# Optimization experiments

Measured on AMD Instinct MI355X. Metric: run time of the kernel, lower is better.

The kernel has to match this reference:

```python
import jax, jax.numpy as jnp
import numpy as np

NSTATE = 1024


def setup_inputs() -> dict:
    key = jax.random.key(0)
    ks = jax.random.split(key, 10)
    b, t = 128, 512
    nalpha, nemb, n = 128, 256, NSTATE
    s = 0.02
    return {
        "x": jax.random.randint(ks[0], (b, t), 0, nalpha),
        "emb": jax.random.normal(ks[1], (nalpha, nemb), jnp.float32) * s,
        "W_fi": jax.random.normal(ks[2], (nemb + 2 * n, 2 * n), jnp.float32) * s,
        "b_fi": jnp.zeros((2 * n,), jnp.float32),
        "W_cu": jax.random.normal(ks[3], (nemb + n, n), jnp.float32) * s,
        "b_cu": jnp.zeros((n,), jnp.float32),
        "W_h": jax.random.normal(ks[4], (nemb + 2 * n, n), jnp.float32) * s,
        "b_h": jnp.zeros((n,), jnp.float32),
        "W_out": jax.random.normal(ks[5], (n, nalpha), jnp.float32) * s,
        "b_out": jnp.zeros((nalpha,), jnp.float32),
    }


def reference(x, emb, W_fi, b_fi, W_cu, b_cu, W_h, b_h, W_out, b_out):
    b, t = x.shape
    n = NSTATE
    f = emb[x]                      # (b, t, nemb) embedding lookup
    f_t = jnp.transpose(f, (1, 0, 2))  # (t, b, nemb) for scan over time

    def step(carry, xt):
        h, c = carry
        ga = jnp.concatenate([xt, h, c], axis=1)        # (b, nemb+2n)
        fi = jax.nn.sigmoid(ga @ W_fi + b_fi)           # (b, 2n) forget|input
        cu = jnp.tanh(jnp.concatenate([xt, h], axis=1) @ W_cu + b_cu)
        c2 = fi[:, :n] * c + fi[:, n:] * cu             # (b, n)
        hg = jnp.concatenate([xt, h, c2], axis=1) @ W_h + b_h  # note: no sigmoid (faithful to source)
        h2 = hg * jnp.tanh(c2)
        return (h2, c2), h2

    init = (jnp.zeros((b, n), f.dtype), jnp.zeros((b, n), f.dtype))
    _, states_t = jax.lax.scan(step, init, f_t)         # (t, b, n)
    states = jnp.transpose(states_t, (1, 0, 2))         # (b, t, n)
    y = states @ W_out + b_out                          # (b, t, nalphabet)
    return y
```

## Files before the change

kernel.cpp:

```cpp
#include <hip/hip_runtime.h>

typedef __attribute__((ext_vector_type(8))) short short8;
typedef __attribute__((ext_vector_type(4))) float f32x4;

#define B_   128
#define T_   512
#define NE_  256
#define N_   1024
#define NA_  128
#define KFI  2304
#define KCU  1280
#define BN   (B_ * N_)
#define TS   513

#define OFF_WTFI   0UL
#define OFF_WTCU   9437184UL
#define OFF_WTH    12058624UL
#define OFF_WTOUT  16777216UL
#define OFF_XE     17039360UL
#define OFF_FLAGS  50593792UL
#define OFF_CBF    50595840UL
#define OFF_STATES 51120128UL

__device__ __forceinline__ unsigned short f2bf(float v) {
  unsigned int u = __float_as_uint(v);
  unsigned int r = (u + 0x7fffu + ((u >> 16) & 1u)) >> 16;
  return (unsigned short)r;
}
__device__ __forceinline__ float sigm(float x) { return 1.f / (1.f + __expf(-x)); }
__device__ __forceinline__ float tanhfast(float x) { return 1.f - 2.f / (__expf(2.f * x) + 1.f); }

#define MFMA(a, b, c) __builtin_amdgcn_mfma_f32_16x16x32_bf16((a), (b), (c), 0, 0, 0)

__device__ __forceinline__ short8 ld8_agent(const unsigned short* p) {
  union { unsigned long long q[2]; short8 v; } u;
  u.q[0] = __hip_atomic_load((unsigned long long*)p,     __ATOMIC_RELAXED, __HIP_MEMORY_SCOPE_AGENT);
  u.q[1] = __hip_atomic_load((unsigned long long*)p + 1, __ATOMIC_RELAXED, __HIP_MEMORY_SCOPE_AGENT);
  return u.v;
}

__global__ void transpose_to_bf16(const float* __restrict__ src,
                                  unsigned short* __restrict__ dst,
                                  int K, int N) {
  __shared__ float tile[32][33];
  const int k0 = blockIdx.y * 32, n0 = blockIdx.x * 32;
  const int tx = threadIdx.x, ty = threadIdx.y;
#pragma unroll
  for (int i = 0; i < 32; i += 8)
    tile[ty + i][tx] = src[(size_t)(k0 + ty + i) * N + n0 + tx];
  __syncthreads();
#pragma unroll
  for (int i = 0; i < 32; i += 8)
    dst[(size_t)(n0 + ty + i) * K + k0 + tx] = f2bf(tile[tx][ty + i]);
}

__global__ void embed_kernel(const int* __restrict__ x, const float* __restrict__ emb,
                             unsigned short* __restrict__ xe) {
  const int r = blockIdx.x;
  const int b = r & 127, t = r >> 7;
  const int e = threadIdx.x;
  const int a = x[b * T_ + t];
  xe[(size_t)r * NE_ + e] = f2bf(emb[(size_t)a * NE_ + e]);
}

__global__ void zero_sync_region(char* __restrict__ ws) {
  unsigned* p = (unsigned*)(ws + OFF_FLAGS);
  const int i = blockIdx.x * blockDim.x + threadIdx.x;
  if (i < (int)((OFF_STATES - OFF_FLAGS) / 4))
    __hip_atomic_store(p + i, 0u, __ATOMIC_RELAXED, __HIP_MEMORY_SCOPE_AGENT);
}

__global__ void zero_h0(char* __restrict__ ws) {
  unsigned* st = (unsigned*)(ws + OFF_STATES);
  unsigned* row = st + (size_t)blockIdx.x * TS * 512;
  __hip_atomic_store(row + threadIdx.x,       0u, __ATOMIC_RELAXED, __HIP_MEMORY_SCOPE_AGENT);
  __hip_atomic_store(row + 256 + threadIdx.x, 0u, __ATOMIC_RELAXED, __HIP_MEMORY_SCOPE_AGENT);
}

__global__ void __launch_bounds__(256) lstm_persistent(
    char* __restrict__ ws,
    const float* __restrict__ b_fi,
    const float* __restrict__ b_cu,
    const float* __restrict__ b_h) {
  const unsigned short* Wt_fi = (const unsigned short*)(ws + OFF_WTFI);
  const unsigned short* Wt_cu = (const unsigned short*)(ws + OFF_WTCU);
  const unsigned short* Wt_h  = (const unsigned short*)(ws + OFF_WTH);
  const unsigned short* xe    = (const unsigned short*)(ws + OFF_XE);
  unsigned short* cbf = (unsigned short*)(ws + OFF_CBF);
  unsigned*       cbf32 = (unsigned*)(ws + OFF_CBF);
  unsigned short* states = (unsigned short*)(ws + OFF_STATES);
  unsigned*       states32 = (unsigned*)(ws + OFF_STATES);
  unsigned* flagsP = (unsigned*)(ws + OFF_FLAGS);
  unsigned* flagsQ = flagsP + 256;

  const int blk  = blockIdx.x;
  const int xcd  = blk & 7;
  const int slot = blk >> 3;
  const int ni   = xcd * 8 + (slot >> 2);
  const int mi   = slot & 3;
  const int tid  = threadIdx.x;
  const int wave = tid >> 6;
  const int lane = tid & 63;
  const int l15  = lane & 15;
  const int quad = lane >> 4;
  const int qo   = quad * 8;
  const int n0   = ni * 16;
  const int mA0  = mi * 32 + l15;
  const int mA1  = mA0 + 16;

  const unsigned short* bfp = Wt_fi + (size_t)(n0 + l15) * KFI;
  const unsigned short* bip = Wt_fi + (size_t)(N_ + n0 + l15) * KFI;
  const unsigned short* bup = Wt_cu + (size_t)(n0 + l15) * KCU;
  const unsigned short* bhp = Wt_h  + (size_t)(n0 + l15) * KFI;

  unsigned* gflagP = flagsP + mi * 64;
  unsigned* gflagQ = flagsQ + mi * 64;

  __shared__ float red[4][6][4][64];
  __shared__ float sb[4][16];
  if (tid < 64) {
    const int g = tid >> 4, col = tid & 15;
    float v;
    if      (g == 0) v = b_fi[n0 + col];
    else if (g == 1) v = b_fi[N_ + n0 + col];
    else if (g == 2) v = b_cu[n0 + col];
    else             v = b_h[n0 + col];
    sb[g][col] = v;
  }

  const int row_l = tid >> 3;
  const int colp  = tid & 7;
  const int gh    = row_l >> 4;
  const int re    = row_l & 3;
  const int lbase = ((row_l >> 2) & 3) * 16 + colp * 2;
  const int me    = mi * 32 + row_l;

  float creg[2] = {0.f, 0.f};

  for (int t = 0; t < T_; ++t) {
    const int cur = t & 1, prv = cur ^ 1;
    const unsigned short* xr0 = xe + ((size_t)t * B_ + mA0) * NE_;
    const unsigned short* xr1 = xe + ((size_t)t * B_ + mA1) * NE_;
    const unsigned short* hr0 = states + ((size_t)mA0 * TS + t) * N_;
    const unsigned short* hr1 = states + ((size_t)mA1 * TS + t) * N_;
    const unsigned short* cr0 = cbf + (size_t)prv * BN + (size_t)mA0 * N_;
    const unsigned short* cr1 = cbf + (size_t)prv * BN + (size_t)mA1 * N_;

    if (wave == 0) {
      const unsigned tgt = (unsigned)t;
      while (__hip_atomic_load(gflagQ + lane, __ATOMIC_RELAXED, __HIP_MEMORY_SCOPE_AGENT) < tgt) { }
    }
    __syncthreads();
    __builtin_amdgcn_fence(__ATOMIC_ACQUIRE, "workgroup");

    short8 axh0[10], axh1[10];
    f32x4 f0 = {0.f,0.f,0.f,0.f}, f1 = {0.f,0.f,0.f,0.f};
    f32x4 i0 = {0.f,0.f,0.f,0.f}, i1 = {0.f,0.f,0.f,0.f};
    f32x4 u0 = {0.f,0.f,0.f,0.f}, u1 = {0.f,0.f,0.f,0.f};
#pragma unroll
    for (int c = 0; c < 10; ++c) {
      const int k = (wave + 4 * c) * 32;
      short8 a0, a1;
      if (c < 2) {
        a0 = *(const short8*)(xr0 + k + qo);
        a1 = *(const short8*)(xr1 + k + qo);
      } else {
        a0 = __builtin_nontemporal_load((const short8*)(hr0 + (k - NE_) + qo));
        a1 = __builtin_nontemporal_load((const short8*)(hr1 + (k - NE_) + qo));
      }
      axh0[c] = a0; axh1[c] = a1;
      short8 bf = *(const short8*)(bfp + k + qo);
      short8 bi = *(const short8*)(bip + k + qo);
      short8 bu = *(const short8*)(bup + k + qo);
      f0 = MFMA(a0, bf, f0);  f1 = MFMA(a1, bf, f1);
      i0 = MFMA(a0, bi, i0);  i1 = MFMA(a1, bi, i1);
      u0 = MFMA(a0, bu, u0);  u1 = MFMA(a1, bu, u1);
    }
#pragma unroll
    for (int c = 10; c < 18; ++c) {
      const int k = (wave + 4 * c) * 32;
      short8 a0 = ld8_agent(cr0 + (k - NE_ - N_) + qo);
      short8 a1 = ld8_agent(cr1 + (k - NE_ - N_) + qo);
      short8 bf = *(const short8*)(bfp + k + qo);
      short8 bi = *(const short8*)(bip + k + qo);
      f0 = MFMA(a0, bf, f0);  f1 = MFMA(a1, bf, f1);
      i0 = MFMA(a0, bi, i0);  i1 = MFMA(a1, bi, i1);
    }
#pragma unroll
    for (int r = 0; r < 4; ++r) {
      red[wave][0][r][lane] = f0[r];  red[wave][1][r][lane] = f1[r];
      red[wave][2][r][lane] = i0[r];  red[wave][3][r][lane] = i1[r];
      red[wave][4][r][lane] = u0[r];  red[wave][5][r][lane] = u1[r];
    }
    __syncthreads();
    {
      unsigned pack = 0;
#pragma unroll
      for (int j = 0; j < 2; ++j) {
        const int L = lbase + j;
        const float fv = red[0][gh][re][L] + red[1][gh][re][L] +
                         red[2][gh][re][L] + red[3][gh][re][L] + sb[0][colp * 2 + j];
        const float iv = red[0][2+gh][re][L] + red[1][2+gh][re][L] +
                         red[2][2+gh][re][L] + red[3][2+gh][re][L] + sb[1][colp * 2 + j];
        const float uv = red[0][4+gh][re][L] + red[1][4+gh][re][L] +
                         red[2][4+gh][re][L] + red[3][4+gh][re][L] + sb[2][colp * 2 + j];
        const float c2v = sigm(fv) * creg[j] + sigm(iv) * tanhfast(uv);
        creg[j] = c2v;
        pack |= (unsigned)f2bf(c2v) << (16 * j);
      }
      unsigned* p = cbf32 + (((size_t)cur * BN + (size_t)me * N_ + n0 + colp * 2) >> 1);
      __hip_atomic_store(p, pack, __ATOMIC_RELAXED, __HIP_MEMORY_SCOPE_AGENT);
    }
    __builtin_amdgcn_fence(__ATOMIC_RELEASE, "workgroup");
    __builtin_amdgcn_s_waitcnt(0);
    __syncthreads();
    if (tid == 0)
      __hip_atomic_store(gflagP + ni, (unsigned)(t + 1), __ATOMIC_RELAXED, __HIP_MEMORY_SCOPE_AGENT);

    f32x4 h0 = {0.f,0.f,0.f,0.f}, h1 = {0.f,0.f,0.f,0.f};
#pragma unroll
    for (int c = 0; c < 10; ++c) {
      const int k = (wave + 4 * c) * 32;
      short8 bh = *(const short8*)(bhp + k + qo);
      h0 = MFMA(axh0[c], bh, h0);
      h1 = MFMA(axh1[c], bh, h1);
    }
    if (wave == 0) {
      const unsigned tgt = (unsigned)(t + 1);
      while (__hip_atomic_load(gflagP + lane, __ATOMIC_RELAXED, __HIP_MEMORY_SCOPE_AGENT) < tgt) { }
    }
    __syncthreads();
    __builtin_amdgcn_fence(__ATOMIC_ACQUIRE, "workgroup");
    const unsigned short* c2r0 = cbf + (size_t)cur * BN + (size_t)mA0 * N_;
    const unsigned short* c2r1 = cbf + (size_t)cur * BN + (size_t)mA1 * N_;
#pragma unroll
    for (int c = 10; c < 18; ++c) {
      const int k = (wave + 4 * c) * 32;
      short8 a0 = ld8_agent(c2r0 + (k - NE_ - N_) + qo);
      short8 a1 = ld8_agent(c2r1 + (k - NE_ - N_) + qo);
      short8 bh = *(const short8*)(bhp + k + qo);
      h0 = MFMA(a0, bh, h0);
      h1 = MFMA(a1, bh, h1);
    }
#pragma unroll
    for (int r = 0; r < 4; ++r) {
      red[wave][0][r][lane] = h0[r];
      red[wave][1][r][lane] = h1[r];
    }
    __syncthreads();
    {
      unsigned pack = 0;
#pragma unroll
      for (int j = 0; j < 2; ++j) {
        const int L = lbase + j;
        const float hv = red[0][gh][re][L] + red[1][gh][re][L] +
                         red[2][gh][re][L] + red[3][gh][re][L] + sb[3][colp * 2 + j];
        const float h2 = hv * tanhfast(creg[j]);
        pack |= (unsigned)f2bf(h2) << (16 * j);
      }
      unsigned* p = states32 + (((size_t)me * TS + t + 1) * N_ + n0 + colp * 2 >> 1);
      __hip_atomic_store(p, pack, __ATOMIC_RELAXED, __HIP_MEMORY_SCOPE_AGENT);
    }
    __builtin_amdgcn_fence(__ATOMIC_RELEASE, "workgroup");
    __builtin_amdgcn_s_waitcnt(0);
    __syncthreads();
    if (tid == 0)
      __hip_atomic_store(gflagQ + ni, (unsigned)(t + 1), __ATOMIC_RELAXED, __HIP_MEMORY_SCOPE_AGENT);
  }
}

__global__ void __launch_bounds__(256) out_gemm(const char* __restrict__ ws,
                                                const float* __restrict__ b_out,
                                                float* __restrict__ y) {
  const unsigned short* states = (const unsigned short*)(ws + OFF_STATES);
  const unsigned short* Wt_out = (const unsigned short*)(ws + OFF_WTOUT);
  const int tid = threadIdx.x, wave = tid >> 6, lane = tid & 63;
  const int l15 = lane & 15, quad = lane >> 4, qo = quad * 8;
  const int msub = wave & 1, npair = wave >> 1;
  const size_t r0 = (size_t)blockIdx.x * 32;
  const size_t mb = r0 >> 9;
  const unsigned short* arow =
      states + (mb * TS + (r0 & 511) + msub * 16 + l15 + 1) * N_;
  const unsigned short* b0p = Wt_out + (size_t)(npair * 64 + 0  + l15) * N_;
  const unsigned short* b1p = Wt_out + (size_t)(npair * 64 + 16 + l15) * N_;
  const unsigned short* b2p = Wt_out + (size_t)(npair * 64 + 32 + l15) * N_;
  const unsigned short* b3p = Wt_out + (size_t)(npair * 64 + 48 + l15) * N_;
  f32x4 a0 = {0.f,0.f,0.f,0.f}, a1 = {0.f,0.f,0.f,0.f};
  f32x4 a2 = {0.f,0.f,0.f,0.f}, a3 = {0.f,0.f,0.f,0.f};
#pragma unroll 8
  for (int c = 0; c < 32; ++c) {
    const int k = c * 32;
    short8 av = *(const short8*)(arow + k + qo);
    a0 = MFMA(av, *(const short8*)(b0p + k + qo), a0);
    a1 = MFMA(av, *(const short8*)(b1p + k + qo), a1);
    a2 = MFMA(av, *(const short8*)(b2p + k + qo), a2);
    a3 = MFMA(av, *(const short8*)(b3p + k + qo), a3);
  }
#pragma unroll
  for (int r = 0; r < 4; ++r) {
    const size_t m = r0 + msub * 16 + quad * 4 + r;
    y[m * NA_ + npair * 64 + 0  + l15] = a0[r] + b_out[npair * 64 + 0  + l15];
    y[m * NA_ + npair * 64 + 16 + l15] = a1[r] + b_out[npair * 64 + 16 + l15];
    y[m * NA_ + npair * 64 + 32 + l15] = a2[r] + b_out[npair * 64 + 32 + l15];
    y[m * NA_ + npair * 64 + 48 + l15] = a3[r] + b_out[npair * 64 + 48 + l15];
  }
}

extern "C" void kernel_launch(void* const* d_in, const int* in_sizes, int n_in,
                              void* d_out, int out_size, void* d_ws, size_t ws_size,
                              hipStream_t stream) {
  const int*   x     = (const int*)d_in[0];
  const float* emb   = (const float*)d_in[1];
  const float* W_fi  = (const float*)d_in[2];
  const float* b_fi  = (const float*)d_in[3];
  const float* W_cu  = (const float*)d_in[4];
  const float* b_cu  = (const float*)d_in[5];
  const float* W_h   = (const float*)d_in[6];
  const float* b_h   = (const float*)d_in[7];
  const float* W_out = (const float*)d_in[8];
  const float* b_out = (const float*)d_in[9];
  char* ws = (char*)d_ws;
  float* y = (float*)d_out;
  (void)in_sizes; (void)n_in; (void)out_size; (void)ws_size;

  transpose_to_bf16<<<dim3(2048 / 32, 2304 / 32), dim3(32, 8), 0, stream>>>(
      W_fi, (unsigned short*)(ws + OFF_WTFI), KFI, 2048);
  transpose_to_bf16<<<dim3(1024 / 32, 1280 / 32), dim3(32, 8), 0, stream>>>(
      W_cu, (unsigned short*)(ws + OFF_WTCU), KCU, 1024);
  transpose_to_bf16<<<dim3(1024 / 32, 2304 / 32), dim3(32, 8), 0, stream>>>(
      W_h, (unsigned short*)(ws + OFF_WTH), KFI, 1024);
  transpose_to_bf16<<<dim3(128 / 32, 1024 / 32), dim3(32, 8), 0, stream>>>(
      W_out, (unsigned short*)(ws + OFF_WTOUT), N_, 128);

  embed_kernel<<<T_ * B_, NE_, 0, stream>>>(x, emb, (unsigned short*)(ws + OFF_XE));

  zero_sync_region<<<514, 256, 0, stream>>>(ws);
  zero_h0<<<128, 256, 0, stream>>>(ws);

  char* wsp = ws;
  void* kargs[4] = { (void*)&wsp, (void*)&b_fi, (void*)&b_cu, (void*)&b_h };
  hipLaunchCooperativeKernel((void*)lstm_persistent, dim3(256), dim3(256),
                             kargs, 0, stream);

  out_gemm<<<(B_ * T_) / 32, 256, 0, stream>>>(ws, b_out, y);
}
```

Baseline: 10.66 ms.

## Split batch into two interleaved 16-row groups to overlap sync waits with compute

Each block now handles two independent 16-row batch groups instead of one 32-row group. It interleaves their P (cell) and Q (hidden) phases, so the MFMA work of one group can run while the other group's flags propagate. Within each phase, the loads that do not depend on the flag (x, c, or h) are issued before the spin-wait, which moves useful work ahead of the synchronization point. The cost is twice as many flag waits and barriers per step with smaller MFMA batches per phase. The explicit acquire/release fences are also removed, which leaves memory-ordering correctness resting on waitcnt and agent-scope atomics.

Result: slower. 17.58 ms (+65.0%).

```diff
diff --git a/kernel.cpp b/kernel.cpp
--- a/kernel.cpp
+++ b/kernel.cpp
@@ -19,8 +19,8 @@
 #define OFF_WTOUT  16777216UL
 #define OFF_XE     17039360UL
 #define OFF_FLAGS  50593792UL
-#define OFF_CBF    50595840UL
-#define OFF_STATES 51120128UL
+#define OFF_CBF    50597888UL
+#define OFF_STATES 51122176UL
 
 __device__ __forceinline__ unsigned short f2bf(float v) {
   unsigned int u = __float_as_uint(v);
@@ -86,18 +86,19 @@
   const unsigned short* Wt_cu = (const unsigned short*)(ws + OFF_WTCU);
   const unsigned short* Wt_h  = (const unsigned short*)(ws + OFF_WTH);
   const unsigned short* xe    = (const unsigned short*)(ws + OFF_XE);
-  unsigned short* cbf = (unsigned short*)(ws + OFF_CBF);
-  unsigned*       cbf32 = (unsigned*)(ws + OFF_CBF);
+  unsigned short* cbf    = (unsigned short*)(ws + OFF_CBF);
+  unsigned*       cbf32  = (unsigned*)(ws + OFF_CBF);
   unsigned short* states = (unsigned short*)(ws + OFF_STATES);
   unsigned*       states32 = (unsigned*)(ws + OFF_STATES);
-  unsigned* flagsP = (unsigned*)(ws + OFF_FLAGS);
-  unsigned* flagsQ = flagsP + 256;
+  unsigned* fP = (unsigned*)(ws + OFF_FLAGS);
+  unsigned* fQ = fP + 512;
 
   const int blk  = blockIdx.x;
   const int xcd  = blk & 7;
-  const int slot = blk >> 3;
-  const int ni   = xcd * 8 + (slot >> 2);
-  const int mi   = slot & 3;
+  const int slot = (blk >> 3) & 3;
+  const int nh   = blk >> 5;
+  const int ni   = xcd * 8 + nh;
+  const int gA   = slot, gB = slot + 4;
   const int tid  = threadIdx.x;
   const int wave = tid >> 6;
   const int lane = tid & 63;
@@ -105,18 +106,13 @@
   const int quad = lane >> 4;
   const int qo   = quad * 8;
   const int n0   = ni * 16;
-  const int mA0  = mi * 32 + l15;
-  const int mA1  = mA0 + 16;
 
   const unsigned short* bfp = Wt_fi + (size_t)(n0 + l15) * KFI;
   const unsigned short* bip = Wt_fi + (size_t)(N_ + n0 + l15) * KFI;
   const unsigned short* bup = Wt_cu + (size_t)(n0 + l15) * KCU;
   const unsigned short* bhp = Wt_h  + (size_t)(n0 + l15) * KFI;
 
-  unsigned* gflagP = flagsP + mi * 64;
-  unsigned* gflagQ = flagsQ + mi * 64;
-
-  __shared__ float red[4][6][4][64];
+  __shared__ float red[4][3][4][72];
   __shared__ float sb[4][16];
   if (tid < 64) {
     const int g = tid >> 4, col = tid & 15;
@@ -128,144 +124,138 @@
     sb[g][col] = v;
   }
 
-  const int row_l = tid >> 3;
-  const int colp  = tid & 7;
-  const int gh    = row_l >> 4;
-  const int re    = row_l & 3;
-  const int lbase = ((row_l >> 2) & 3) * 16 + colp * 2;
-  const int me    = mi * 32 + row_l;
-
-  float creg[2] = {0.f, 0.f};
+  const int erow = tid >> 3;
+  const int colp = tid & 7;
+  const int ereg = erow & 3;
+  const int lbas = (erow >> 2) * 16 + colp * 2;
+
+  float cA[2] = {0.f, 0.f}, cB[2] = {0.f, 0.f};
+
+  auto phaseP = [&](const int g, const int t, float* cv) {
+    const int cur = t & 1, prv = cur ^ 1;
+    const unsigned short* xr = xe + ((size_t)t * B_ + g * 16 + l15) * NE_;
+    const unsigned short* hr = states + ((size_t)(g * 16 + l15) * TS + t) * N_;
+    const unsigned short* cr = cbf + (size_t)prv * BN + (size_t)(g * 16 + l15) * N_;
+    f32x4 fa = {0.f,0.f,0.f,0.f}, ia = {0.f,0.f,0.f,0.f}, ua = {0.f,0.f,0.f,0.f};
+#pragma unroll
+    for (int c = 0; c < 2; ++c) {
+      const int k = (wave + 4 * c) * 32;
+      short8 a = *(const short8*)(xr + k + qo);
+      fa = MFMA(a, *(const short8*)(bfp + k + qo), fa);
+      ia = MFMA(a, *(const short8*)(bip + k + qo), ia);
+      ua = MFMA(a, *(const short8*)(bup + k + qo), ua);
+    }
+#pragma unroll
+    for (int c = 10; c < 18; ++c) {
+      const int k = (wave + 4 * c) * 32;
+      short8 a = ld8_agent(cr + (k - KCU) + qo);
+      fa = MFMA(a, *(const short8*)(bfp + k + qo), fa);
+      ia = MFMA(a, *(const short8*)(bip + k + qo), ia);
+    }
+    if (wave == 0) {
+      while (__hip_atomic_load(fQ + g * 64 + lane, __ATOMIC_RELAXED,
+                               __HIP_MEMORY_SCOPE_AGENT) < (unsigned)t) { }
+    }
+    __syncthreads();
+#pragma unroll
+    for (int c = 2; c < 10; ++c) {
+      const int k = (wave + 4 * c) * 32;
+      short8 a = __builtin_nontemporal_load((const short8*)(hr + (k - NE_) + qo));
+      fa = MFMA(a, *(const short8*)(bfp + k + qo), fa);
+      ia = MFMA(a, *(const short8*)(bip + k + qo), ia);
+      ua = MFMA(a, *(const short8*)(bup + k + qo), ua);
+    }
+#pragma unroll
+    for (int r = 0; r < 4; ++r) {
+      red[wave][0][r][lane] = fa[r];
+      red[wave][1][r][lane] = ia[r];
+      red[wave][2][r][lane] = ua[r];
+    }
+    __syncthreads();
+    if (tid < 128) {
+      unsigned pack = 0;
+#pragma unroll
+      for (int j = 0; j < 2; ++j) {
+        const int L = lbas + j;
+        const float fv = red[0][0][ereg][L] + red[1][0][ereg][L] +
+                         red[2][0][ereg][L] + red[3][0][ereg][L] + sb[0][colp * 2 + j];
+        const float iv = red[0][1][ereg][L] + red[1][1][ereg][L] +
+                         red[2][1][ereg][L] + red[3][1][ereg][L] + sb[1][colp * 2 + j];
+        const float uv = red[0][2][ereg][L] + red[1][2][ereg][L] +
+                         red[2][2][ereg][L] + red[3][2][ereg][L] + sb[2][colp * 2 + j];
+        const float c2 = sigm(fv) * cv[j] + sigm(iv) * tanhfast(uv);
+        cv[j] = c2;
+        pack |= (unsigned)f2bf(c2) << (16 * j);
+      }
+      unsigned* p = cbf32 +
+          (((size_t)cur * BN + (size_t)(g * 16 + erow) * N_ + n0 + colp * 2) >> 1);
+      __hip_atomic_store(p, pack, __ATOMIC_RELAXED, __HIP_MEMORY_SCOPE_AGENT);
+    }
+    __builtin_amdgcn_s_waitcnt(0);
+    __syncthreads();
+    if (tid == 0)
+      __hip_atomic_store(fP + g * 64 + ni, (unsigned)(t + 1), __ATOMIC_RELAXED,
+                         __HIP_MEMORY_SCOPE_AGENT);
+  };
+
+  auto phaseQ = [&](const int g, const int t, const float* cv) {
+    const int cur = t & 1;
+    const unsigned short* xr = xe + ((size_t)t * B_ + g * 16 + l15) * NE_;
+    const unsigned short* hr = states + ((size_t)(g * 16 + l15) * TS + t) * N_;
+    const unsigned short* c2r = cbf + (size_t)cur * BN + (size_t)(g * 16 + l15) * N_;
+    f32x4 ha = {0.f,0.f,0.f,0.f};
+#pragma unroll
+    for (int c = 0; c < 2; ++c) {
+      const int k = (wave + 4 * c) * 32;
+      short8 a = *(const short8*)(xr + k + qo);
+      ha = MFMA(a, *(const short8*)(bhp + k + qo), ha);
+    }
+#pragma unroll
+    for (int c = 2; c < 10; ++c) {
+      const int k = (wave + 4 * c) * 32;
+      short8 a = __builtin_nontemporal_load((const short8*)(hr + (k - NE_) + qo));
+      ha = MFMA(a, *(const short8*)(bhp + k + qo), ha);
+    }
+    if (wave == 0) {
+      while (__hip_atomic_load(fP + g * 64 + lane, __ATOMIC_RELAXED,
+                               __HIP_MEMORY_SCOPE_AGENT) < (unsigned)(t + 1)) { }
+    }
+    __syncthreads();
+#pragma unroll
+    for (int c = 10; c < 18; ++c) {
+      const int k = (wave + 4 * c) * 32;
+      short8 a = ld8_agent(c2r + (k - KCU) + qo);
+      ha = MFMA(a, *(const short8*)(bhp + k + qo), ha);
+    }
+#pragma unroll
+    for (int r = 0; r < 4; ++r)
+      red[wave][0][r][lane] = ha[r];
+    __syncthreads();
+    if (tid < 128) {
+      unsigned pack = 0;
+#pragma unroll
+      for (int j = 0; j < 2; ++j) {
+        const int L = lbas + j;
+        const float hv = red[0][0][ereg][L] + red[1][0][ereg][L] +
+                         red[2][0][ereg][L] + red[3][0][ereg][L] + sb[3][colp * 2 + j];
+        pack |= (unsigned)f2bf(hv * tanhfast(cv[j])) << (16 * j);
+      }
+      unsigned* p = states32 +
+          ((((size_t)(g * 16 + erow) * TS + (t + 1)) * N_ + n0 + colp * 2) >> 1);
+      __hip_atomic_store(p, pack, __ATOMIC_RELAXED, __HIP_MEMORY_SCOPE_AGENT);
+    }
+    __builtin_amdgcn_s_waitcnt(0);
+    __syncthreads();
+    if (tid == 0)
+      __hip_atomic_store(fQ + g * 64 + ni, (unsigned)(t + 1), __ATOMIC_RELAXED,
+                         __HIP_MEMORY_SCOPE_AGENT);
+  };
 
   for (int t = 0; t < T_; ++t) {
-    const int cur = t & 1, prv = cur ^ 1;
-    const unsigned short* xr0 = xe + ((size_t)t * B_ + mA0) * NE_;
-    const unsigned short* xr1 = xe + ((size_t)t * B_ + mA1) * NE_;
-    const unsigned short* hr0 = states + ((size_t)mA0 * TS + t) * N_;
-    const unsigned short* hr1 = states + ((size_t)mA1 * TS + t) * N_;
-    const unsigned short* cr0 = cbf + (size_t)prv * BN + (size_t)mA0 * N_;
-    const unsigned short* cr1 = cbf + (size_t)prv * BN + (size_t)mA1 * N_;
-
-    if (wave == 0) {
-      const unsigned tgt = (unsigned)t;
-      while (__hip_atomic_load(gflagQ + lane, __ATOMIC_RELAXED, __HIP_MEMORY_SCOPE_AGENT) < tgt) { }
-    }
-    __syncthreads();
-    __builtin_amdgcn_fence(__ATOMIC_ACQUIRE, "workgroup");
-
-    short8 axh0[10], axh1[10];
-    f32x4 f0 = {0.f,0.f,0.f,0.f}, f1 = {0.f,0.f,0.f,0.f};
-    f32x4 i0 = {0.f,0.f,0.f,0.f}, i1 = {0.f,0.f,0.f,0.f};
-    f32x4 u0 = {0.f,0.f,0.f,0.f}, u1 = {0.f,0.f,0.f,0.f};
-#pragma unroll
-    for (int c = 0; c < 10; ++c) {
-      const int k = (wave + 4 * c) * 32;
-      short8 a0, a1;
-      if (c < 2) {
-        a0 = *(const short8*)(xr0 + k + qo);
-        a1 = *(const short8*)(xr1 + k + qo);
-      } else {
-        a0 = __builtin_nontemporal_load((const short8*)(hr0 + (k - NE_) + qo));
-        a1 = __builtin_nontemporal_load((const short8*)(hr1 + (k - NE_) + qo));
-      }
-      axh0[c] = a0; axh1[c] = a1;
-      short8 bf = *(const short8*)(bfp + k + qo);
-      short8 bi = *(const short8*)(bip + k + qo);
-      short8 bu = *(const short8*)(bup + k + qo);
-      f0 = MFMA(a0, bf, f0);  f1 = MFMA(a1, bf, f1);
-      i0 = MFMA(a0, bi, i0);  i1 = MFMA(a1, bi, i1);
-      u0 = MFMA(a0, bu, u0);  u1 = MFMA(a1, bu, u1);
-    }
-#pragma unroll
-    for (int c = 10; c < 18; ++c) {
-      const int k = (wave + 4 * c) * 32;
-      short8 a0 = ld8_agent(cr0 + (k - NE_ - N_) + qo);
-      short8 a1 = ld8_agent(cr1 + (k - NE_ - N_) + qo);
-      short8 bf = *(const short8*)(bfp + k + qo);
-      short8 bi = *(const short8*)(bip + k + qo);
-      f0 = MFMA(a0, bf, f0);  f1 = MFMA(a1, bf, f1);
-      i0 = MFMA(a0, bi, i0);  i1 = MFMA(a1, bi, i1);
-    }
-#pragma unroll
-    for (int r = 0; r < 4; ++r) {
-      red[wave][0][r][lane] = f0[r];  red[wave][1][r][lane] = f1[r];
-      red[wave][2][r][lane] = i0[r];  red[wave][3][r][lane] = i1[r];
-      red[wave][4][r][lane] = u0[r];  red[wave][5][r][lane] = u1[r];
-    }
-    __syncthreads();
-    {
-      unsigned pack = 0;
-#pragma unroll
-      for (int j = 0; j < 2; ++j) {
-        const int L = lbase + j;
-        const float fv = red[0][gh][re][L] + red[1][gh][re][L] +
-                         red[2][gh][re][L] + red[3][gh][re][L] + sb[0][colp * 2 + j];
-        const float iv = red[0][2+gh][re][L] + red[1][2+gh][re][L] +
-                         red[2][2+gh][re][L] + red[3][2+gh][re][L] + sb[1][colp * 2 + j];
-        const float uv = red[0][4+gh][re][L] + red[1][4+gh][re][L] +
-                         red[2][4+gh][re][L] + red[3][4+gh][re][L] + sb[2][colp * 2 + j];
-        const float c2v = sigm(fv) * creg[j] + sigm(iv) * tanhfast(uv);
-        creg[j] = c2v;
-        pack |= (unsigned)f2bf(c2v) << (16 * j);
-      }
-      unsigned* p = cbf32 + (((size_t)cur * BN + (size_t)me * N_ + n0 + colp * 2) >> 1);
-      __hip_atomic_store(p, pack, __ATOMIC_RELAXED, __HIP_MEMORY_SCOPE_AGENT);
-    }
-    __builtin_amdgcn_fence(__ATOMIC_RELEASE, "workgroup");
-    __builtin_amdgcn_s_waitcnt(0);
-    __syncthreads();
-    if (tid == 0)
-      __hip_atomic_store(gflagP + ni, (unsigned)(t + 1), __ATOMIC_RELAXED, __HIP_MEMORY_SCOPE_AGENT);
-
-    f32x4 h0 = {0.f,0.f,0.f,0.f}, h1 = {0.f,0.f,0.f,0.f};
-#pragma unroll
-    for (int c = 0; c < 10; ++c) {
-      const int k = (wave + 4 * c) * 32;
-      short8 bh = *(const short8*)(bhp + k + qo);
-      h0 = MFMA(axh0[c], bh, h0);
-      h1 = MFMA(axh1[c], bh, h1);
-    }
-    if (wave == 0) {
-      const unsigned tgt = (unsigned)(t + 1);
-      while (__hip_atomic_load(gflagP + lane, __ATOMIC_RELAXED, __HIP_MEMORY_SCOPE_AGENT) < tgt) { }
-    }
-    __syncthreads();
-    __builtin_amdgcn_fence(__ATOMIC_ACQUIRE, "workgroup");
-    const unsigned short* c2r0 = cbf + (size_t)cur * BN + (size_t)mA0 * N_;
-    const unsigned short* c2r1 = cbf + (size_t)cur * BN + (size_t)mA1 * N_;
-#pragma unroll
-    for (int c = 10; c < 18; ++c) {
-      const int k = (wave + 4 * c) * 32;
-      short8 a0 = ld8_agent(c2r0 + (k - NE_ - N_) + qo);
-      short8 a1 = ld8_agent(c2r1 + (k - NE_ - N_) + qo);
-      short8 bh = *(const short8*)(bhp + k + qo);
-      h0 = MFMA(a0, bh, h0);
-      h1 = MFMA(a1, bh, h1);
-    }
-#pragma unroll
-    for (int r = 0; r < 4; ++r) {
-      red[wave][0][r][lane] = h0[r];
-      red[wave][1][r][lane] = h1[r];
-    }
-    __syncthreads();
-    {
-      unsigned pack = 0;
-#pragma unroll
-      for (int j = 0; j < 2; ++j) {
-        const int L = lbase + j;
-        const float hv = red[0][gh][re][L] + red[1][gh][re][L] +
-                         red[2][gh][re][L] + red[3][gh][re][L] + sb[3][colp * 2 + j];
-        const float h2 = hv * tanhfast(creg[j]);
-        pack |= (unsigned)f2bf(h2) << (16 * j);
-      }
-      unsigned* p = states32 + (((size_t)me * TS + t + 1) * N_ + n0 + colp * 2 >> 1);
-      __hip_atomic_store(p, pack, __ATOMIC_RELAXED, __HIP_MEMORY_SCOPE_AGENT);
-    }
-    __builtin_amdgcn_fence(__ATOMIC_RELEASE, "workgroup");
-    __builtin_amdgcn_s_waitcnt(0);
-    __syncthreads();
-    if (tid == 0)
-      __hip_atomic_store(gflagQ + ni, (unsigned)(t + 1), __ATOMIC_RELAXED, __HIP_MEMORY_SCOPE_AGENT);
+    phaseP(gA, t, cA);
+    phaseP(gB, t, cB);
+    phaseQ(gA, t, cA);
+    phaseQ(gB, t, cB);
   }
 }
 
@@ -334,7 +324,7 @@
 
   embed_kernel<<<T_ * B_, NE_, 0, stream>>>(x, emb, (unsigned short*)(ws + OFF_XE));
 
-  zero_sync_region<<<514, 256, 0, stream>>>(ws);
+  zero_sync_region<<<516, 256, 0, stream>>>(ws);
   zero_h0<<<128, 256, 0, stream>>>(ws);
 
   char* wsp = ws;
```

## Carry c-contribution of forget/input gates across steps and overlap x-projection with barrier wait

Applied to the files above, without the earlier changes.

The c2 @ W_fi partial products for the next step's forget/input gates are now computed in the h-phase of the current step, reusing the c2 operands already loaded, and carried into the next iteration. Each step's gate phase therefore no longer reloads the c buffer. The x-embedding MFMAs are issued before spinning on the h-ready flag so they overlap the inter-block wait. The spin uses wave-wide __all, the explicit acquire/release fences are removed, and the LDS reduction array is padded to 72 to reduce bank conflicts. Dropping the fences risks memory-ordering issues on the cross-block flags.

Measured after the change: 8.543 ms. -19.9%, faster.

```diff
diff --git a/kernel.cpp b/kernel.cpp
--- a/kernel.cpp
+++ b/kernel.cpp
@@ -20,7 +20,7 @@
 #define OFF_XE     17039360UL
 #define OFF_FLAGS  50593792UL
 #define OFF_CBF    50595840UL
-#define OFF_STATES 51120128UL
+#define OFF_STATES 51122176UL
 
 __device__ __forceinline__ unsigned short f2bf(float v) {
   unsigned int u = __float_as_uint(v);
@@ -86,18 +86,19 @@
   const unsigned short* Wt_cu = (const unsigned short*)(ws + OFF_WTCU);
   const unsigned short* Wt_h  = (const unsigned short*)(ws + OFF_WTH);
   const unsigned short* xe    = (const unsigned short*)(ws + OFF_XE);
-  unsigned short* cbf = (unsigned short*)(ws + OFF_CBF);
-  unsigned*       cbf32 = (unsigned*)(ws + OFF_CBF);
+  unsigned short* cbf    = (unsigned short*)(ws + OFF_CBF);
+  unsigned*       cbf32  = (unsigned*)(ws + OFF_CBF);
   unsigned short* states = (unsigned short*)(ws + OFF_STATES);
   unsigned*       states32 = (unsigned*)(ws + OFF_STATES);
-  unsigned* flagsP = (unsigned*)(ws + OFF_FLAGS);
-  unsigned* flagsQ = flagsP + 256;
+  unsigned* aP = (unsigned*)(ws + OFF_FLAGS);
+  unsigned* aQ = aP + 256;
 
   const int blk  = blockIdx.x;
   const int xcd  = blk & 7;
   const int slot = blk >> 3;
-  const int ni   = xcd * 8 + (slot >> 2);
+  const int nh   = slot >> 2;
   const int mi   = slot & 3;
+  const int ni   = xcd * 8 + nh;
   const int tid  = threadIdx.x;
   const int wave = tid >> 6;
   const int lane = tid & 63;
@@ -113,10 +114,7 @@
   const unsigned short* bup = Wt_cu + (size_t)(n0 + l15) * KCU;
   const unsigned short* bhp = Wt_h  + (size_t)(n0 + l15) * KFI;
 
-  unsigned* gflagP = flagsP + mi * 64;
-  unsigned* gflagQ = flagsQ + mi * 64;
-
-  __shared__ float red[4][6][4][64];
+  __shared__ float red[4][6][4][72];
   __shared__ float sb[4][16];
   if (tid < 64) {
     const int g = tid >> 4, col = tid & 15;
@@ -128,63 +126,56 @@
     sb[g][col] = v;
   }
 
-  const int row_l = tid >> 3;
-  const int colp  = tid & 7;
-  const int gh    = row_l >> 4;
-  const int re    = row_l & 3;
-  const int lbase = ((row_l >> 2) & 3) * 16 + colp * 2;
-  const int me    = mi * 32 + row_l;
+  const int hh   = tid >> 7;
+  const int erow = (tid >> 3) & 15;
+  const int colp = tid & 7;
+  const int ereg = erow & 3;
+  const int lbas = (erow >> 2) * 16 + colp * 2;
+  const int brow = mi * 32 + hh * 16 + erow;
 
   float creg[2] = {0.f, 0.f};
+  f32x4 fc0 = {0,0,0,0}, fc1 = {0,0,0,0};
+  f32x4 ic0 = {0,0,0,0}, ic1 = {0,0,0,0};
 
   for (int t = 0; t < T_; ++t) {
-    const int cur = t & 1, prv = cur ^ 1;
+    const int cur = t & 1;
     const unsigned short* xr0 = xe + ((size_t)t * B_ + mA0) * NE_;
     const unsigned short* xr1 = xe + ((size_t)t * B_ + mA1) * NE_;
     const unsigned short* hr0 = states + ((size_t)mA0 * TS + t) * N_;
     const unsigned short* hr1 = states + ((size_t)mA1 * TS + t) * N_;
-    const unsigned short* cr0 = cbf + (size_t)prv * BN + (size_t)mA0 * N_;
-    const unsigned short* cr1 = cbf + (size_t)prv * BN + (size_t)mA1 * N_;
-
-    if (wave == 0) {
-      const unsigned tgt = (unsigned)t;
-      while (__hip_atomic_load(gflagQ + lane, __ATOMIC_RELAXED, __HIP_MEMORY_SCOPE_AGENT) < tgt) { }
-    }
-    __syncthreads();
-    __builtin_amdgcn_fence(__ATOMIC_ACQUIRE, "workgroup");
-
-    short8 axh0[10], axh1[10];
-    f32x4 f0 = {0.f,0.f,0.f,0.f}, f1 = {0.f,0.f,0.f,0.f};
-    f32x4 i0 = {0.f,0.f,0.f,0.f}, i1 = {0.f,0.f,0.f,0.f};
-    f32x4 u0 = {0.f,0.f,0.f,0.f}, u1 = {0.f,0.f,0.f,0.f};
-#pragma unroll
-    for (int c = 0; c < 10; ++c) {
+
+    f32x4 f0 = fc0, f1 = fc1, i0 = ic0, i1 = ic1;
+    f32x4 u0 = {0,0,0,0}, u1 = {0,0,0,0};
+    short8 ax0[2], ax1[2], axh0[8], axh1[8];
+#pragma unroll
+    for (int c = 0; c < 2; ++c) {
       const int k = (wave + 4 * c) * 32;
-      short8 a0, a1;
-      if (c < 2) {
-        a0 = *(const short8*)(xr0 + k + qo);
-        a1 = *(const short8*)(xr1 + k + qo);
-      } else {
-        a0 = __builtin_nontemporal_load((const short8*)(hr0 + (k - NE_) + qo));
-        a1 = __builtin_nontemporal_load((const short8*)(hr1 + (k - NE_) + qo));
-      }
-      axh0[c] = a0; axh1[c] = a1;
+      ax0[c] = *(const short8*)(xr0 + k + qo);
+      ax1[c] = *(const short8*)(xr1 + k + qo);
       short8 bf = *(const short8*)(bfp + k + qo);
       short8 bi = *(const short8*)(bip + k + qo);
       short8 bu = *(const short8*)(bup + k + qo);
-      f0 = MFMA(a0, bf, f0);  f1 = MFMA(a1, bf, f1);
-      i0 = MFMA(a0, bi, i0);  i1 = MFMA(a1, bi, i1);
-      u0 = MFMA(a0, bu, u0);  u1 = MFMA(a1, bu, u1);
-    }
-#pragma unroll
-    for (int c = 10; c < 18; ++c) {
-      const int k = (wave + 4 * c) * 32;
-      short8 a0 = ld8_agent(cr0 + (k - NE_ - N_) + qo);
-      short8 a1 = ld8_agent(cr1 + (k - NE_ - N_) + qo);
+      f0 = MFMA(ax0[c], bf, f0);  f1 = MFMA(ax1[c], bf, f1);
+      i0 = MFMA(ax0[c], bi, i0);  i1 = MFMA(ax1[c], bi, i1);
+      u0 = MFMA(ax0[c], bu, u0);  u1 = MFMA(ax1[c], bu, u1);
+    }
+    if (wave == 0) {
+      while (!__all((int)(__hip_atomic_load(aQ + mi * 64 + lane, __ATOMIC_RELAXED,
+                                            __HIP_MEMORY_SCOPE_AGENT) >= (unsigned)t))) { }
+    }
+    __syncthreads();
+#pragma unroll
+    for (int c = 0; c < 8; ++c) {
+      const int k = (wave + 4 * (c + 2)) * 32;
+      const int kh = k - NE_;
+      axh0[c] = *(const short8*)(hr0 + kh + qo);
+      axh1[c] = *(const short8*)(hr1 + kh + qo);
       short8 bf = *(const short8*)(bfp + k + qo);
       short8 bi = *(const short8*)(bip + k + qo);
-      f0 = MFMA(a0, bf, f0);  f1 = MFMA(a1, bf, f1);
-      i0 = MFMA(a0, bi, i0);  i1 = MFMA(a1, bi, i1);
+      short8 bu = *(const short8*)(bup + k + qo);
+      f0 = MFMA(axh0[c], bf, f0);  f1 = MFMA(axh1[c], bf, f1);
+      i0 = MFMA(axh0[c], bi, i0);  i1 = MFMA(axh1[c], bi, i1);
+      u0 = MFMA(axh0[c], bu, u0);  u1 = MFMA(axh1[c], bu, u1);
     }
 #pragma unroll
     for (int r = 0; r < 4; ++r) {
@@ -197,50 +188,60 @@
       unsigned pack = 0;
 #pragma unroll
       for (int j = 0; j < 2; ++j) {
-        const int L = lbase + j;
-        const float fv = red[0][gh][re][L] + red[1][gh][re][L] +
-                         red[2][gh][re][L] + red[3][gh][re][L] + sb[0][colp * 2 + j];
-        const float iv = red[0][2+gh][re][L] + red[1][2+gh][re][L] +
-                         red[2][2+gh][re][L] + red[3][2+gh][re][L] + sb[1][colp * 2 + j];
-        const float uv = red[0][4+gh][re][L] + red[1][4+gh][re][L] +
-                         red[2][4+gh][re][L] + red[3][4+gh][re][L] + sb[2][colp * 2 + j];
-        const float c2v = sigm(fv) * creg[j] + sigm(iv) * tanhfast(uv);
-        creg[j] = c2v;
-        pack |= (unsigned)f2bf(c2v) << (16 * j);
+        const int L = lbas + j;
+        const float fv = red[0][hh][ereg][L] + red[1][hh][ereg][L] +
+                         red[2][hh][ereg][L] + red[3][hh][ereg][L] + sb[0][colp * 2 + j];
+        const float iv = red[0][2+hh][ereg][L] + red[1][2+hh][ereg][L] +
+                         red[2][2+hh][ereg][L] + red[3][2+hh][ereg][L] + sb[1][colp * 2 + j];
+        const float uv = red[0][4+hh][ereg][L] + red[1][4+hh][ereg][L] +
+                         red[2][4+hh][ereg][L] + red[3][4+hh][ereg][L] + sb[2][colp * 2 + j];
+        const float c2 = sigm(fv) * creg[j] + sigm(iv) * tanhfast(uv);
+        creg[j] = c2;
+        pack |= (unsigned)f2bf(c2) << (16 * j);
       }
-      unsigned* p = cbf32 + (((size_t)cur * BN + (size_t)me * N_ + n0 + colp * 2) >> 1);
+      unsigned* p = cbf32 +
+          (((size_t)cur * BN + (size_t)brow * N_ + n0 + colp * 2) >> 1);
       __hip_atomic_store(p, pack, __ATOMIC_RELAXED, __HIP_MEMORY_SCOPE_AGENT);
     }
-    __builtin_amdgcn_fence(__ATOMIC_RELEASE, "workgroup");
     __builtin_amdgcn_s_waitcnt(0);
     __syncthreads();
     if (tid == 0)
-      __hip_atomic_store(gflagP + ni, (unsigned)(t + 1), __ATOMIC_RELAXED, __HIP_MEMORY_SCOPE_AGENT);
-
-    f32x4 h0 = {0.f,0.f,0.f,0.f}, h1 = {0.f,0.f,0.f,0.f};
-#pragma unroll
-    for (int c = 0; c < 10; ++c) {
+      __hip_atomic_store(aP + mi * 64 + ni, (unsigned)(t + 1), __ATOMIC_RELAXED,
+                         __HIP_MEMORY_SCOPE_AGENT);
+
+    f32x4 h0 = {0,0,0,0}, h1 = {0,0,0,0};
+    f32x4 fn0 = {0,0,0,0}, fn1 = {0,0,0,0}, in0 = {0,0,0,0}, in1 = {0,0,0,0};
+#pragma unroll
+    for (int c = 0; c < 2; ++c) {
       const int k = (wave + 4 * c) * 32;
       short8 bh = *(const short8*)(bhp + k + qo);
-      h0 = MFMA(axh0[c], bh, h0);
-      h1 = MFMA(axh1[c], bh, h1);
+      h0 = MFMA(ax0[c], bh, h0);  h1 = MFMA(ax1[c], bh, h1);
+    }
+#pragma unroll
+    for (int c = 0; c < 8; ++c) {
+      const int k = (wave + 4 * (c + 2)) * 32;
+      short8 bh = *(const short8*)(bhp + k + qo);
+      h0 = MFMA(axh0[c], bh, h0);  h1 = MFMA(axh1[c], bh, h1);
     }
     if (wave == 0) {
-      const unsigned tgt = (unsigned)(t + 1);
-      while (__hip_atomic_load(gflagP + lane, __ATOMIC_RELAXED, __HIP_MEMORY_SCOPE_AGENT) < tgt) { }
-    }
-    __syncthreads();
-    __builtin_amdgcn_fence(__ATOMIC_ACQUIRE, "workgroup");
+      while (!__all((int)(__hip_atomic_load(aP + mi * 64 + lane, __ATOMIC_RELAXED,
+                                            __HIP_MEMORY_SCOPE_AGENT) >= (unsigned)(t + 1)))) { }
+    }
+    __syncthreads();
     const unsigned short* c2r0 = cbf + (size_t)cur * BN + (size_t)mA0 * N_;
     const unsigned short* c2r1 = cbf + (size_t)cur * BN + (size_t)mA1 * N_;
 #pragma unroll
-    for (int c = 10; c < 18; ++c) {
-      const int k = (wave + 4 * c) * 32;
-      short8 a0 = ld8_agent(c2r0 + (k - NE_ - N_) + qo);
-      short8 a1 = ld8_agent(c2r1 + (k - NE_ - N_) + qo);
+    for (int c = 0; c < 8; ++c) {
+      const int k = (wave + 4 * (c + 10)) * 32;
+      const int kc = k - KCU;
+      short8 ca0 = ld8_agent(c2r0 + kc + qo);
+      short8 ca1 = ld8_agent(c2r1 + kc + qo);
       short8 bh = *(const short8*)(bhp + k + qo);
-      h0 = MFMA(a0, bh, h0);
-      h1 = MFMA(a1, bh, h1);
+      short8 bf = *(const short8*)(bfp + k + qo);
+      short8 bi = *(const short8*)(bip + k + qo);
+      h0  = MFMA(ca0, bh, h0);   h1  = MFMA(ca1, bh, h1);
+      fn0 = MFMA(ca0, bf, fn0);  fn1 = MFMA(ca1, bf, fn1);
+      in0 = MFMA(ca0, bi, in0);  in1 = MFMA(ca1, bi, in1);
     }
 #pragma unroll
     for (int r = 0; r < 4; ++r) {
@@ -252,20 +253,22 @@
       unsigned pack = 0;
 #pragma unroll
       for (int j = 0; j < 2; ++j) {
-        const int L = lbase + j;
-        const float hv = red[0][gh][re][L] + red[1][gh][re][L] +
-                         red[2][gh][re][L] + red[3][gh][re][L] + sb[3][colp * 2 + j];
-        const float h2 = hv * tanhfast(creg[j]);
-        pack |= (unsigned)f2bf(h2) << (16 * j);
+        const int L = lbas + j;
+        const float hv = red[0][hh][ereg][L] + red[1][hh][ereg][L] +
+                         red[2][hh][ereg][L] + red[3][hh][ereg][L] + sb[3][colp * 2 + j];
+        pack |= (unsigned)f2bf(hv * tanhfast(creg[j])) << (16 * j);
       }
-      unsigned* p = states32 + (((size_t)me * TS + t + 1) * N_ + n0 + colp * 2 >> 1);
+      unsigned* p = states32 +
+          ((((size_t)brow * TS + (t + 1)) * N_ + n0 + colp * 2) >> 1);
       __hip_atomic_store(p, pack, __ATOMIC_RELAXED, __HIP_MEMORY_SCOPE_AGENT);
     }
-    __builtin_amdgcn_fence(__ATOMIC_RELEASE, "workgroup");
     __builtin_amdgcn_s_waitcnt(0);
     __syncthreads();
     if (tid == 0)
-      __hip_atomic_store(gflagQ + ni, (unsigned)(t + 1), __ATOMIC_RELAXED, __HIP_MEMORY_SCOPE_AGENT);
+      __hip_atomic_store(aQ + mi * 64 + ni, (unsigned)(t + 1), __ATOMIC_RELAXED,
+                         __HIP_MEMORY_SCOPE_AGENT);
+
+    fc0 = fn0; fc1 = fn1; ic0 = in0; ic1 = in1;
   }
 }
 
@@ -334,7 +337,7 @@
 
   embed_kernel<<<T_ * B_, NE_, 0, stream>>>(x, emb, (unsigned short*)(ws + OFF_XE));
 
-  zero_sync_region<<<514, 256, 0, stream>>>(ws);
+  zero_sync_region<<<516, 256, 0, stream>>>(ws);
   zero_h0<<<128, 256, 0, stream>>>(ws);
 
   char* wsp = ws;
```
